# Kernel optimization log

Measured on AMD Instinct MI355X. Metric: run time of the kernel, lower is better.

Reference implementation:

```python
import jax, jax.numpy as jnp
import numpy as np

GRID_SIZE = 5
SPLINE_ORDER = 3
GRID_RANGE = (-1.0, 1.0)
IN_FEATURES = 1024
OUT_FEATURES = 1024
NUM_BASIS = GRID_SIZE + SPLINE_ORDER  # 8
SCALE_BASE = 1.0
SCALE_SPLINE = 1.0

_h = (GRID_RANGE[1] - GRID_RANGE[0]) / GRID_SIZE
_GRID = np.linspace(GRID_RANGE[0] - SPLINE_ORDER * _h,
                    GRID_RANGE[1] + SPLINE_ORDER * _h,
                    GRID_SIZE + 2 * SPLINE_ORDER + 1).astype(np.float32)  # (12,)


def bspline_basis(x, grid):
    # x: (B, I)  ->  basis: (B, I, NUM_BASIS)
    x = jnp.clip(x, GRID_RANGE[0], GRID_RANGE[1])
    xg = x[..., None]                              # (B, I, 1)
    g = grid                                       # (G,) broadcasts over (B, I)
    basis = ((xg >= g[:-1]) & (xg < g[1:])).astype(x.dtype)  # (B, I, G-1)
    for k in range(1, SPLINE_ORDER + 1):
        left_den = g[k:-1] - g[:-(k + 1)]
        left_den = jnp.where(left_den == 0, jnp.ones_like(left_den), left_den)
        right_den = g[k + 1:] - g[1:-k]
        right_den = jnp.where(right_den == 0, jnp.ones_like(right_den), right_den)
        left = (xg - g[:-(k + 1)]) / left_den * basis[..., :-1]
        right = (g[k + 1:] - xg) / right_den * basis[..., 1:]
        basis = left + right
    return basis


def setup_inputs() -> dict:
    key = jax.random.key(0)
    k1, k2, k3 = jax.random.split(key, 3)
    x = jax.random.normal(k1, (8192, IN_FEATURES), dtype=jnp.float32)
    base_weight = jax.random.normal(k2, (OUT_FEATURES, IN_FEATURES), dtype=jnp.float32) * 0.03
    spline_weight = jax.random.normal(k3, (OUT_FEATURES, IN_FEATURES, NUM_BASIS), dtype=jnp.float32) * 0.03
    return {"x": x, "base_weight": base_weight, "spline_weight": spline_weight}


def reference(x, base_weight, spline_weight):
    grid = jnp.asarray(_GRID, dtype=x.dtype)
    # base branch: SiLU(x) @ W_base^T
    base_out = jax.nn.silu(x) @ base_weight.T              # (B, O)
    base_out = base_out * SCALE_BASE
    # spline branch: einsum over (in, basis)
    basis = bspline_basis(x, grid)                         # (B, I, K)
    spline_out = jnp.einsum('bik,oik->bo', basis, spline_weight)
    spline_out = spline_out * SCALE_SPLINE
    return base_out + spline_out
```

## Files before the change

### kernel.cpp

```cpp
#include <hip/hip_runtime.h>
#include <hip/hip_bf16.h>
#include <cstdint>


typedef short s16x8 __attribute__((ext_vector_type(8)));
typedef float f32x4 __attribute__((ext_vector_type(4)));

#define GK 9216
#define GN 1024
#define GI 1024
#define GM 8192

#define BK 32
#define KSPLIT 4608
#define NT 144

#define BS_BLK 32768
#define RP_BLK 4608

__device__ __forceinline__ void cp16(const __hip_bfloat16* g, __hip_bfloat16* l) {
  __builtin_amdgcn_global_load_lds((const __attribute__((address_space(1))) void*)g,
                                   (__attribute__((address_space(3))) void*)l, 16, 0, 0);
}

__device__ __forceinline__ uint32_t bfbits(float f) {
  __hip_bfloat16 h = __float2bfloat16(f);
  unsigned short us;
  __builtin_memcpy(&us, &h, 2);
  return (uint32_t)us;
}

__device__ __forceinline__ void basis4(float xv, int& jj, float& w0, float& w1,
                                       float& w2, float& w3) {
  float t = fminf(1.f, fmaxf(-1.f, xv));
  float us = (t + 1.f) * 2.5f;
  int j = (int)us;
  if (j > 4) j = 4;
  float u = us - (float)j;
  float u2 = u * u, u3 = u2 * u;
  float om = 1.f - u;
  jj = j;
  w0 = om * om * om * (1.f / 6.f);
  w1 = (3.f * u3 - 6.f * u2 + 4.f) * (1.f / 6.f);
  w2 = (-3.f * u3 + 3.f * u2 + 3.f * u + 1.f) * (1.f / 6.f);
  w3 = u3 * (1.f / 6.f);
}

__global__ void kan_prep_all(const float* __restrict__ x,
                             const float* __restrict__ baseW,
                             const float* __restrict__ splineW,
                             __hip_bfloat16* __restrict__ W2,
                             __hip_bfloat16* __restrict__ A) {
  int bid = blockIdx.x;
  if (bid < BS_BLK) {
    int t = bid * 256 + threadIdx.x;
    int b = t >> 10, i = t & 1023;
    float xv = x[t];

    float sl = xv / (1.f + __expf(-xv));
    A[(size_t)b * GK + 8192 + i] = __float2bfloat16(sl);

    int jj; float w0, w1, w2, w3;
    basis4(xv, jj, w0, w1, w2, w3);
    uint64_t W64 = (uint64_t)(bfbits(w0) | (bfbits(w1) << 16)) |
                   ((uint64_t)(bfbits(w2) | (bfbits(w3) << 16)) << 32);
    int sh = jj * 16;
    uint64_t lo = (jj < 4) ? (W64 << sh) : 0ull;
    uint64_t hi = (jj == 0) ? 0ull : (W64 >> (64 - sh));
    uint4 pk;
    pk.x = (uint32_t)lo;  pk.y = (uint32_t)(lo >> 32);
    pk.z = (uint32_t)hi;  pk.w = (uint32_t)(hi >> 32);
    *(uint4*)(A + (size_t)b * GK + (size_t)i * 8) = pk;
  } else {
    int t = (bid - BS_BLK) * 256 + threadIdx.x;
    int o = t / 1152;
    int c = (t - o * 1152) * 8;
    const float* src = (c < 8192) ? (splineW + (size_t)o * 8192 + c)
                                  : (baseW + (size_t)o * GI + (c - 8192));
    float4 v0 = ((const float4*)src)[0];
    float4 v1 = ((const float4*)src)[1];
    uint4 pk;
    pk.x = bfbits(v0.x) | (bfbits(v0.y) << 16);
    pk.y = bfbits(v0.z) | (bfbits(v0.w) << 16);
    pk.z = bfbits(v1.x) | (bfbits(v1.y) << 16);
    pk.w = bfbits(v1.z) | (bfbits(v1.w) << 16);
    *(uint4*)(W2 + (size_t)o * GK + c) = pk;
  }
}

__global__ __launch_bounds__(512, 2) void kan_gemm8(
    const __hip_bfloat16* __restrict__ A,
    const __hip_bfloat16* __restrict__ B,
    float* __restrict__ C0,
    float* __restrict__ C1) {
  __shared__ __align__(16) __hip_bfloat16 As[3][256 * BK];
  __shared__ __align__(16) __hip_bfloat16 Bs[3][256 * BK];
  const int tid = threadIdx.x;
  const int lane = tid & 63;
  const int wave = tid >> 6;
  const int wm = wave >> 2, wn = wave & 3;

  const int linear = (blockIdx.z * 32 + blockIdx.y) * 4 + blockIdx.x;
  const int c = (linear & 7) * 32 + (linear >> 3);
  const int colBand = c & 3;
  const int rowBand = (c >> 2) & 31;
  const int ks = c >> 7;
  const int blockRow = rowBand * 256;
  const int blockCol = colBand * 256;
  const int kbase = ks * KSPLIT;

  const int srow = tid >> 2;
  const int sq = tid & 3;
  const __hip_bfloat16* aSrc = A + (size_t)(blockRow + srow) * GK + kbase + sq * 8;
  const __hip_bfloat16* bSrc = B + (size_t)(blockCol + srow) * GK + kbase + sq * 8;
  const int ldsOff = wave * 512;

#define STAGE(T, BUF)                                             \
  do {                                                            \
    const __hip_bfloat16* ga = aSrc + (T) * BK;                   \
    const __hip_bfloat16* gb = bSrc + (T) * BK;                   \
    cp16(ga, As[BUF] + ldsOff);                                   \
    cp16(ga + 128 * GK, As[BUF] + ldsOff + 4096);                 \
    cp16(gb, Bs[BUF] + ldsOff);                                   \
    cp16(gb + 128 * GK, Bs[BUF] + ldsOff + 4096);                 \
  } while (0)

  const int q = lane >> 4, r16 = lane & 15;
  const int aBase = (wm * 128 + r16) * 4 + q;
  const int bBase = (wn * 64 + r16) * 4 + q;

  f32x4 acc[8][4] = {};

  STAGE(0, 0);
  __builtin_amdgcn_sched_barrier(0);
  STAGE(1, 1);
  __builtin_amdgcn_sched_barrier(0);
  STAGE(2, 2);
  __builtin_amdgcn_sched_barrier(0);
  asm volatile("s_waitcnt vmcnt(8)" ::: "memory");
  __builtin_amdgcn_sched_barrier(0);
  __builtin_amdgcn_s_barrier();

  for (int t3 = 0; t3 < NT / 3; ++t3) {
#pragma unroll
    for (int u = 0; u < 3; ++u) {
      const int t = t3 * 3 + u;
      const int tp = (t + 3 < NT) ? (t + 3) : 0;
      __builtin_amdgcn_sched_barrier(0);
      const s16x8* Af = (const s16x8*)As[u];
      const s16x8* Bf = (const s16x8*)Bs[u];
      s16x8 af[8], bfg[4];
#pragma unroll
      for (int tm = 0; tm < 8; ++tm) af[tm] = Af[aBase + tm * 64];
#pragma unroll
      for (int tn = 0; tn < 4; ++tn) bfg[tn] = Bf[bBase + tn * 64];
      asm volatile("s_waitcnt lgkmcnt(0)" ::: "memory");
      __builtin_amdgcn_sched_barrier(0);
      __builtin_amdgcn_s_barrier();
      __builtin_amdgcn_sched_barrier(0);
      STAGE(tp, u);
      __builtin_amdgcn_sched_barrier(0);
      __builtin_amdgcn_s_setprio(1);
#pragma unroll
      for (int tm = 0; tm < 8; ++tm)
#pragma unroll
        for (int tn = 0; tn < 4; ++tn)
          acc[tm][tn] = __builtin_amdgcn_mfma_f32_16x16x32_bf16(
              af[tm], bfg[tn], acc[tm][tn], 0, 0, 0);
      __builtin_amdgcn_s_setprio(0);
      asm volatile("s_waitcnt vmcnt(8)" ::: "memory");
      __builtin_amdgcn_sched_barrier(0);
      __builtin_amdgcn_s_barrier();
    }
  }
  asm volatile("s_waitcnt vmcnt(0)" ::: "memory");

  float* __restrict__ Cd = ks ? C1 : C0;
  const int cRow0 = blockRow + wm * 128 + q * 4;
  const int cCol0 = blockCol + wn * 64 + r16;
#pragma unroll
  for (int tm = 0; tm < 8; ++tm)
#pragma unroll
    for (int tn = 0; tn < 4; ++tn) {
      int col = cCol0 + tn * 16;
      size_t base = (size_t)(cRow0 + tm * 16) * GN + col;
#pragma unroll
      for (int r = 0; r < 4; ++r)
        Cd[base + (size_t)r * GN] = acc[tm][tn][r];
    }
#undef STAGE
}

__global__ void kan_reduce(float* __restrict__ out, const float* __restrict__ part) {
  size_t i = ((size_t)blockIdx.x * 256 + threadIdx.x) * 4;
  float4 a = *(const float4*)(out + i);
  float4 b = *(const float4*)(part + i);
  a.x += b.x; a.y += b.y; a.z += b.z; a.w += b.w;
  *(float4*)(out + i) = a;
}

__global__ __launch_bounds__(512) void kan_gemm(
    const __hip_bfloat16* __restrict__ A,
    const __hip_bfloat16* __restrict__ B,
    float* __restrict__ C) {
  __shared__ __align__(16) __hip_bfloat16 Asf[2][128 * 32];
  __shared__ __align__(16) __hip_bfloat16 Bsf[2][128 * 32];
  const int tid = threadIdx.x;
  const int lane = tid & 63;
  const int wave = tid >> 6;
  const int wm = wave >> 2, wn = wave & 3;

  const int linear = blockIdx.y * 8 + blockIdx.x;
  const int rowBand = (linear & 7) * 8 + ((linear >> 3) & 7);
  const int colBand = linear >> 6;
  const int blockRow = rowBand * 128;
  const int blockCol = colBand * 128;

  const __hip_bfloat16* aPtr = A + (size_t)(blockRow + (tid >> 2)) * GK + (tid & 3) * 8;
  const __hip_bfloat16* bPtr = B + (size_t)(blockCol + (tid >> 2)) * GK + (tid & 3) * 8;
  __hip_bfloat16* ldsA0 = Asf[0] + wave * 512;
  __hip_bfloat16* ldsA1 = Asf[1] + wave * 512;
  __hip_bfloat16* ldsB0 = Bsf[0] + wave * 512;
  __hip_bfloat16* ldsB1 = Bsf[1] + wave * 512;

  f32x4 acc[4][2] = {};

  const int q = lane >> 4;
  const int r16 = lane & 15;
  const int aRow = wm * 64 + r16;
  const int bRow = wn * 32 + r16;

  for (int kt = 0; kt < GK / 64; ++kt) {
    cp16(aPtr, ldsA0);
    cp16(aPtr + 32, ldsA1);
    cp16(bPtr, ldsB0);
    cp16(bPtr + 32, ldsB1);
    aPtr += 64; bPtr += 64;
    __syncthreads();

#pragma unroll
    for (int s = 0; s < 2; ++s) {
      const s16x8* Af = (const s16x8*)Asf[s];
      const s16x8* Bf = (const s16x8*)Bsf[s];
      s16x8 af[4], bfg[2];
#pragma unroll
      for (int tm = 0; tm < 4; ++tm) af[tm] = Af[(aRow + tm * 16) * 4 + q];
#pragma unroll
      for (int tn = 0; tn < 2; ++tn) bfg[tn] = Bf[(bRow + tn * 16) * 4 + q];
#pragma unroll
      for (int tm = 0; tm < 4; ++tm)
#pragma unroll
        for (int tn = 0; tn < 2; ++tn)
          acc[tm][tn] = __builtin_amdgcn_mfma_f32_16x16x32_bf16(
              af[tm], bfg[tn], acc[tm][tn], 0, 0, 0);
    }
    __syncthreads();
  }

  const int cRow0 = blockRow + wm * 64 + q * 4;
  const int cCol0 = blockCol + wn * 32 + r16;
#pragma unroll
  for (int tm = 0; tm < 4; ++tm)
#pragma unroll
    for (int tn = 0; tn < 2; ++tn) {
      int col = cCol0 + tn * 16;
#pragma unroll
      for (int r = 0; r < 4; ++r) {
        int row = cRow0 + tm * 16 + r;
        C[(size_t)row * GN + col] = acc[tm][tn][r];
      }
    }
}

__global__ void kan_naive(const float* __restrict__ x,
                          const float* __restrict__ bw,
                          const float* __restrict__ sw,
                          float* __restrict__ out) {
  int o = blockIdx.x * 256 + threadIdx.x;
  int b = blockIdx.y;
  float acc = 0.f;
  for (int i = 0; i < GI; ++i) {
    float xv = x[(size_t)b * GI + i];
    float sl = xv / (1.f + __expf(-xv));
    acc += sl * bw[(size_t)o * GI + i];
    int jj; float w0, w1, w2, w3;
    basis4(xv, jj, w0, w1, w2, w3);
    const float* swr = sw + ((size_t)o * GI + i) * 8 + jj;
    acc += w0 * swr[0] + w1 * swr[1] + w2 * swr[2] + w3 * swr[3];
  }
  out[(size_t)b * GN + o] = acc;
}

extern "C" void kernel_launch(void* const* d_in, const int* in_sizes, int n_in,
                              void* d_out, int out_size, void* d_ws, size_t ws_size,
                              hipStream_t stream) {
  const float* x  = (const float*)d_in[0];
  const float* bw = (const float*)d_in[1];
  const float* sw = (const float*)d_in[2];
  float* out = (float*)d_out;

  const size_t wBytes = (size_t)GK * GN * 2;
  const size_t aBytes = (size_t)GM * GK * 2;
  const size_t pBytes = (size_t)GM * GN * 4;

  if (ws_size < wBytes + aBytes) {
    kan_naive<<<dim3(GN / 256, GM), 256, 0, stream>>>(x, bw, sw, out);
    return;
  }

  __hip_bfloat16* W2 = (__hip_bfloat16*)d_ws;
  __hip_bfloat16* Abuf = W2 + (size_t)GK * GN;

  kan_prep_all<<<BS_BLK + RP_BLK, 256, 0, stream>>>(x, bw, sw, W2, Abuf);

  if (ws_size >= wBytes + aBytes + pBytes) {
    float* partial = (float*)((char*)d_ws + wBytes + aBytes);
    kan_gemm8<<<dim3(4, 32, 2), 512, 0, stream>>>(Abuf, W2, out, partial);
    kan_reduce<<<GM * GN / (256 * 4), 256, 0, stream>>>(out, partial);
  } else {
    kan_gemm<<<dim3(GN / 128, GM / 128), 512, 0, stream>>>(Abuf, W2, out);
  }
}
```

Before: 296.3 us.

## Replace split-K 256x256 GEMM with 128x256 tiles and swizzled LDS layout

Drops the two-way split-K GEMM and its partial-sum reduce kernel. In their place is a single full-K GEMM with 128x256 block tiles over a 64x4 grid, using fewer accumulators and occupancy hint 4. It also XOR-swizzles the 16-byte chunk index in the global-to-LDS copy and the fragment reads to reduce LDS bank conflicts. This removes the partial-buffer write, the reduce pass and the extra launch, but the smaller A tile lowers operand reuse per block.

```diff
diff --git a/kernel.cpp b/kernel.cpp
--- a/kernel.cpp
+++ b/kernel.cpp
@@ -12,8 +12,7 @@
 #define GM 8192
 
 #define BK 32
-#define KSPLIT 4608
-#define NT 144
+#define NT 288
 
 #define BS_BLK 32768
 #define RP_BLK 4608
@@ -88,31 +87,29 @@
   }
 }
 
-__global__ __launch_bounds__(512, 2) void kan_gemm8(
+__global__ __launch_bounds__(512, 4) void kan_gemm_bc(
     const __hip_bfloat16* __restrict__ A,
     const __hip_bfloat16* __restrict__ B,
-    float* __restrict__ C0,
-    float* __restrict__ C1) {
-  __shared__ __align__(16) __hip_bfloat16 As[3][256 * BK];
+    float* __restrict__ C) {
+  __shared__ __align__(16) __hip_bfloat16 As[3][128 * BK];
   __shared__ __align__(16) __hip_bfloat16 Bs[3][256 * BK];
   const int tid = threadIdx.x;
   const int lane = tid & 63;
   const int wave = tid >> 6;
   const int wm = wave >> 2, wn = wave & 3;
 
-  const int linear = (blockIdx.z * 32 + blockIdx.y) * 4 + blockIdx.x;
+  const int linear = blockIdx.y * 4 + blockIdx.x;
   const int c = (linear & 7) * 32 + (linear >> 3);
   const int colBand = c & 3;
-  const int rowBand = (c >> 2) & 31;
-  const int ks = c >> 7;
-  const int blockRow = rowBand * 256;
+  const int rowBand = c >> 2;
+  const int blockRow = rowBand * 128;
   const int blockCol = colBand * 256;
-  const int kbase = ks * KSPLIT;
 
   const int srow = tid >> 2;
   const int sq = tid & 3;
-  const __hip_bfloat16* aSrc = A + (size_t)(blockRow + srow) * GK + kbase + sq * 8;
-  const __hip_bfloat16* bSrc = B + (size_t)(blockCol + srow) * GK + kbase + sq * 8;
+  const int ssw = sq ^ ((srow >> 1) & 3);
+  const __hip_bfloat16* aSrc = A + (size_t)(blockRow + srow) * GK + ssw * 8;
+  const __hip_bfloat16* bSrc = B + (size_t)(blockCol + srow) * GK + ssw * 8;
   const int ldsOff = wave * 512;
 
 #define STAGE(T, BUF)                                             \
@@ -120,16 +117,16 @@
     const __hip_bfloat16* ga = aSrc + (T) * BK;                   \
     const __hip_bfloat16* gb = bSrc + (T) * BK;                   \
     cp16(ga, As[BUF] + ldsOff);                                   \
-    cp16(ga + 128 * GK, As[BUF] + ldsOff + 4096);                 \
     cp16(gb, Bs[BUF] + ldsOff);                                   \
     cp16(gb + 128 * GK, Bs[BUF] + ldsOff + 4096);                 \
   } while (0)
 
   const int q = lane >> 4, r16 = lane & 15;
-  const int aBase = (wm * 128 + r16) * 4 + q;
-  const int bBase = (wn * 64 + r16) * 4 + q;
-
-  f32x4 acc[8][4] = {};
+  const int qs = q ^ ((r16 >> 1) & 3);
+  const int aBase = (wm * 64 + r16) * 4 + qs;
+  const int bBase = (wn * 64 + r16) * 4 + qs;
+
+  f32x4 acc[4][4] = {};
 
   STAGE(0, 0);
   __builtin_amdgcn_sched_barrier(0);
@@ -137,7 +134,7 @@
   __builtin_amdgcn_sched_barrier(0);
   STAGE(2, 2);
   __builtin_amdgcn_sched_barrier(0);
-  asm volatile("s_waitcnt vmcnt(8)" ::: "memory");
+  asm volatile("s_waitcnt vmcnt(6)" ::: "memory");
   __builtin_amdgcn_sched_barrier(0);
   __builtin_amdgcn_s_barrier();
 
@@ -149,9 +146,9 @@
       __builtin_amdgcn_sched_barrier(0);
       const s16x8* Af = (const s16x8*)As[u];
       const s16x8* Bf = (const s16x8*)Bs[u];
-      s16x8 af[8], bfg[4];
-#pragma unroll
-      for (int tm = 0; tm < 8; ++tm) af[tm] = Af[aBase + tm * 64];
+      s16x8 af[4], bfg[4];
+#pragma unroll
+      for (int tm = 0; tm < 4; ++tm) af[tm] = Af[aBase + tm * 64];
 #pragma unroll
       for (int tn = 0; tn < 4; ++tn) bfg[tn] = Bf[bBase + tn * 64];
       asm volatile("s_waitcnt lgkmcnt(0)" ::: "memory");
@@ -162,114 +159,32 @@
       __builtin_amdgcn_sched_barrier(0);
       __builtin_amdgcn_s_setprio(1);
 #pragma unroll
-      for (int tm = 0; tm < 8; ++tm)
+      for (int tm = 0; tm < 4; ++tm)
 #pragma unroll
         for (int tn = 0; tn < 4; ++tn)
           acc[tm][tn] = __builtin_amdgcn_mfma_f32_16x16x32_bf16(
               af[tm], bfg[tn], acc[tm][tn], 0, 0, 0);
       __builtin_amdgcn_s_setprio(0);
-      asm volatile("s_waitcnt vmcnt(8)" ::: "memory");
+      asm volatile("s_waitcnt vmcnt(6)" ::: "memory");
       __builtin_amdgcn_sched_barrier(0);
       __builtin_amdgcn_s_barrier();
     }
   }
   asm volatile("s_waitcnt vmcnt(0)" ::: "memory");
 
-  float* __restrict__ Cd = ks ? C1 : C0;
-  const int cRow0 = blockRow + wm * 128 + q * 4;
+  const int cRow0 = blockRow + wm * 64 + q * 4;
   const int cCol0 = blockCol + wn * 64 + r16;
 #pragma unroll
-  for (int tm = 0; tm < 8; ++tm)
+  for (int tm = 0; tm < 4; ++tm)
 #pragma unroll
     for (int tn = 0; tn < 4; ++tn) {
       int col = cCol0 + tn * 16;
       size_t base = (size_t)(cRow0 + tm * 16) * GN + col;
 #pragma unroll
       for (int r = 0; r < 4; ++r)
-        Cd[base + (size_t)r * GN] = acc[tm][tn][r];
+        C[base + (size_t)r * GN] = acc[tm][tn][r];
     }
 #undef STAGE
-}
-
-__global__ void kan_reduce(float* __restrict__ out, const float* __restrict__ part) {
-  size_t i = ((size_t)blockIdx.x * 256 + threadIdx.x) * 4;
-  float4 a = *(const float4*)(out + i);
-  float4 b = *(const float4*)(part + i);
-  a.x += b.x; a.y += b.y; a.z += b.z; a.w += b.w;
-  *(float4*)(out + i) = a;
-}
-
-__global__ __launch_bounds__(512) void kan_gemm(
-    const __hip_bfloat16* __restrict__ A,
-    const __hip_bfloat16* __restrict__ B,
-    float* __restrict__ C) {
-  __shared__ __align__(16) __hip_bfloat16 Asf[2][128 * 32];
-  __shared__ __align__(16) __hip_bfloat16 Bsf[2][128 * 32];
-  const int tid = threadIdx.x;
-  const int lane = tid & 63;
-  const int wave = tid >> 6;
-  const int wm = wave >> 2, wn = wave & 3;
-
-  const int linear = blockIdx.y * 8 + blockIdx.x;
-  const int rowBand = (linear & 7) * 8 + ((linear >> 3) & 7);
-  const int colBand = linear >> 6;
-  const int blockRow = rowBand * 128;
-  const int blockCol = colBand * 128;
-
-  const __hip_bfloat16* aPtr = A + (size_t)(blockRow + (tid >> 2)) * GK + (tid & 3) * 8;
-  const __hip_bfloat16* bPtr = B + (size_t)(blockCol + (tid >> 2)) * GK + (tid & 3) * 8;
-  __hip_bfloat16* ldsA0 = Asf[0] + wave * 512;
-  __hip_bfloat16* ldsA1 = Asf[1] + wave * 512;
-  __hip_bfloat16* ldsB0 = Bsf[0] + wave * 512;
-  __hip_bfloat16* ldsB1 = Bsf[1] + wave * 512;
-
-  f32x4 acc[4][2] = {};
-
-  const int q = lane >> 4;
-  const int r16 = lane & 15;
-  const int aRow = wm * 64 + r16;
-  const int bRow = wn * 32 + r16;
-
-  for (int kt = 0; kt < GK / 64; ++kt) {
-    cp16(aPtr, ldsA0);
-    cp16(aPtr + 32, ldsA1);
-    cp16(bPtr, ldsB0);
-    cp16(bPtr + 32, ldsB1);
-    aPtr += 64; bPtr += 64;
-    __syncthreads();
-
-#pragma unroll
-    for (int s = 0; s < 2; ++s) {
-      const s16x8* Af = (const s16x8*)Asf[s];
-      const s16x8* Bf = (const s16x8*)Bsf[s];
-      s16x8 af[4], bfg[2];
-#pragma unroll
-      for (int tm = 0; tm < 4; ++tm) af[tm] = Af[(aRow + tm * 16) * 4 + q];
-#pragma unroll
-      for (int tn = 0; tn < 2; ++tn) bfg[tn] = Bf[(bRow + tn * 16) * 4 + q];
-#pragma unroll
-      for (int tm = 0; tm < 4; ++tm)
-#pragma unroll
-        for (int tn = 0; tn < 2; ++tn)
-          acc[tm][tn] = __builtin_amdgcn_mfma_f32_16x16x32_bf16(
-              af[tm], bfg[tn], acc[tm][tn], 0, 0, 0);
-    }
-    __syncthreads();
-  }
-
-  const int cRow0 = blockRow + wm * 64 + q * 4;
-  const int cCol0 = blockCol + wn * 32 + r16;
-#pragma unroll
-  for (int tm = 0; tm < 4; ++tm)
-#pragma unroll
-    for (int tn = 0; tn < 2; ++tn) {
-      int col = cCol0 + tn * 16;
-#pragma unroll
-      for (int r = 0; r < 4; ++r) {
-        int row = cRow0 + tm * 16 + r;
-        C[(size_t)row * GN + col] = acc[tm][tn][r];
-      }
-    }
 }
 
 __global__ void kan_naive(const float* __restrict__ x,
@@ -301,7 +216,6 @@
 
   const size_t wBytes = (size_t)GK * GN * 2;
   const size_t aBytes = (size_t)GM * GK * 2;
-  const size_t pBytes = (size_t)GM * GN * 4;
 
   if (ws_size < wBytes + aBytes) {
     kan_naive<<<dim3(GN / 256, GM), 256, 0, stream>>>(x, bw, sw, out);
@@ -312,12 +226,5 @@
   __hip_bfloat16* Abuf = W2 + (size_t)GK * GN;
 
   kan_prep_all<<<BS_BLK + RP_BLK, 256, 0, stream>>>(x, bw, sw, W2, Abuf);
-
-  if (ws_size >= wBytes + aBytes + pBytes) {
-    float* partial = (float*)((char*)d_ws + wBytes + aBytes);
-    kan_gemm8<<<dim3(4, 32, 2), 512, 0, stream>>>(Abuf, W2, out, partial);
-    kan_reduce<<<GM * GN / (256 * 4), 256, 0, stream>>>(out, partial);
-  } else {
-    kan_gemm<<<dim3(GN / 128, GM / 128), 512, 0, stream>>>(Abuf, W2, out);
-  }
-}
+  kan_gemm_bc<<<dim3(4, 64), 512, 0, stream>>>(Abuf, W2, out);
+}
```

New measurement: 315.6 us. +6.5%, slower.
